# Kernel tuning notes

Hardware: AMD Instinct MI355X
Metric: run time of the kernel (lower is better)

Reference implementation:

```python
import math
import jax, jax.numpy as jnp
import numpy as np

D_MODEL = 1024
D_K = 64
D_V = 64
N_HEADS = 16
D_HIDDEN = 4096
EPS = 1e-5


def setup_inputs() -> dict:
    key = jax.random.key(0)
    ks = jax.random.split(key, 10)
    s = 0.02
    x = jax.random.normal(ks[0], (2, 2048, D_MODEL), dtype=jnp.float32)
    wq = jax.random.normal(ks[1], (D_MODEL, D_K * N_HEADS), jnp.float32) * s
    bq = jnp.zeros((D_K * N_HEADS,), jnp.float32)
    wk = jax.random.normal(ks[2], (D_MODEL, D_K * N_HEADS), jnp.float32) * s
    bk = jnp.zeros((D_K * N_HEADS,), jnp.float32)
    wv = jax.random.normal(ks[3], (D_MODEL, D_V * N_HEADS), jnp.float32) * s
    bv = jnp.zeros((D_V * N_HEADS,), jnp.float32)
    wo = jax.random.normal(ks[4], (D_V * N_HEADS, D_MODEL), jnp.float32) * s
    ln1_g = jnp.ones((D_MODEL,), jnp.float32)
    ln1_b = jnp.zeros((D_MODEL,), jnp.float32)
    w1 = jax.random.normal(ks[5], (D_MODEL, D_HIDDEN), jnp.float32) * s
    b1 = jnp.zeros((D_HIDDEN,), jnp.float32)
    w2 = jax.random.normal(ks[6], (D_HIDDEN, D_MODEL), jnp.float32) * s
    ln2_g = jnp.ones((D_MODEL,), jnp.float32)
    ln2_b = jnp.zeros((D_MODEL,), jnp.float32)
    return dict(x=x, wq=wq, bq=bq, wk=wk, bk=bk, wv=wv, bv=bv, wo=wo,
                ln1_g=ln1_g, ln1_b=ln1_b, w1=w1, b1=b1, w2=w2,
                ln2_g=ln2_g, ln2_b=ln2_b)


def _layernorm(x, g, b):
    mu = jnp.mean(x, axis=-1, keepdims=True)
    var = jnp.mean((x - mu) ** 2, axis=-1, keepdims=True)
    return (x - mu) * jax.lax.rsqrt(var + EPS) * g + b


def reference(x, wq, bq, wk, bk, wv, bv, wo, ln1_g, ln1_b, w1, b1, w2, ln2_g, ln2_b):
    B, S, _ = x.shape
    split = lambda t, d: t.reshape(B, S, N_HEADS, d).transpose(0, 2, 1, 3)  # [B,H,S,d]
    Q = split(x @ wq + bq, D_K)
    K = split(x @ wk + bk, D_K)
    V = split(x @ wv + bv, D_V)
    scores = jnp.einsum('bhqd,bhkd->bhqk', Q / math.sqrt(D_K), K)
    causal = jnp.tril(jnp.ones((S, S), dtype=bool))
    scores = jnp.where(causal, scores, -jnp.inf)
    attn = jax.nn.softmax(scores, axis=-1)
    ctx = jnp.einsum('bhqk,bhkd->bhqd', attn, V)  # [B,H,S,d_v]
    merged = ctx.transpose(0, 2, 1, 3).reshape(B, S, N_HEADS * D_V)
    x = x + _layernorm(merged @ wo, ln1_g, ln1_b)
    h = jax.nn.gelu(x @ w1 + b1, approximate=False)
    x = x + _layernorm(h @ w2, ln2_g, ln2_b)
    return x
```

## Files before the change

### kernel.cpp

```cpp
#include <hip/hip_runtime.h>
#include <math.h>

typedef __bf16 bf16;
typedef __bf16 bf16x4 __attribute__((ext_vector_type(4)));
typedef __bf16 bf16x8 __attribute__((ext_vector_type(8)));
typedef float f32x4 __attribute__((ext_vector_type(4)));

#define MFMA16(a, b, c) __builtin_amdgcn_mfma_f32_16x16x32_bf16(a, b, c, 0, 0, 0)
#define QSCALE 0.180336879f
#define SSTR 3072
#define SOFT_M -14.0f

typedef __attribute__((address_space(3))) unsigned int lds_uint;
typedef const __attribute__((address_space(1))) unsigned int glb_uint;
__device__ __forceinline__ void gload_lds16(const void* g, void* l) {
    __builtin_amdgcn_global_load_lds((glb_uint*)g, (lds_uint*)l, 16, 0, 0);
}
__device__ __forceinline__ unsigned lds_addr(const void* p) {
    return (unsigned)(unsigned long long)(lds_uint*)p;
}

__global__ __launch_bounds__(256) void prep_kernel(
    const float* __restrict__ x,
    const float* __restrict__ wq, const float* __restrict__ wk,
    const float* __restrict__ wv, const float* __restrict__ wo,
    const float* __restrict__ w1, const float* __restrict__ w2,
    const float* __restrict__ bq, const float* __restrict__ bk,
    const float* __restrict__ bv,
    bf16* __restrict__ xbf, bf16* __restrict__ wqkvt, bf16* __restrict__ wot,
    bf16* __restrict__ w1t, bf16* __restrict__ w2t, float* __restrict__ bqkv) {
    const int bid = blockIdx.x, tid = threadIdx.x;
    if (bid < 4096) {
        size_t i = ((size_t)bid * 256 + tid) * 4;
        float4 v = *(const float4*)(x + i);
        bf16x4 o = {(bf16)v.x, (bf16)v.y, (bf16)v.z, (bf16)v.w};
        *(bf16x4*)(xbf + i) = o;
        return;
    }
    if (bid < 16384) {
        __shared__ float tile[32][33];
        const float* W; bf16* Wt; int K, N, n0, k0;
        if (bid < 8192) {
            int l = bid - 4096, z = l >> 10, t = l & 1023;
            W = z == 0 ? wq : z == 1 ? wk : z == 2 ? wv : wo;
            Wt = z == 3 ? wot : wqkvt + (size_t)z * 1024 * 1024;
            K = 1024; N = 1024; n0 = (t & 31) * 32; k0 = (t >> 5) * 32;
        } else if (bid < 12288) {
            int l = bid - 8192;
            W = w1; Wt = w1t; K = 1024; N = 4096;
            n0 = (l & 127) * 32; k0 = (l >> 7) * 32;
        } else {
            int l = bid - 12288;
            W = w2; Wt = w2t; K = 4096; N = 1024;
            n0 = (l & 31) * 32; k0 = (l >> 5) * 32;
        }
        const int tx = tid & 31, ty = tid >> 5;
        for (int i = 0; i < 32; i += 8)
            tile[ty + i][tx] = W[(size_t)(k0 + ty + i) * N + n0 + tx];
        __syncthreads();
        for (int i = 0; i < 32; i += 8)
            Wt[(size_t)(n0 + ty + i) * K + k0 + tx] = (bf16)tile[tx][ty + i];
        return;
    }
    int i = (bid - 16384) * 256 + tid;
    bqkv[i] = i < 1024 ? bq[i] : i < 2048 ? bk[i - 1024] : bv[i - 2048];
}

__global__ void transpose_v_kernel(const bf16* __restrict__ QKV, bf16* __restrict__ Vtg) {
    __shared__ bf16 t[64 * 64];
    const int tid = threadIdx.x;
    const int st = blockIdx.x;
    const int bh = blockIdx.y;
    const int b = bh >> 4, h = bh & 15;
    const bf16* src = QKV + (size_t)b * 2048 * SSTR + 2048 + h * 64 + (size_t)st * 64 * SSTR;
    const int s = tid >> 3, oct = tid & 7;
    bf16x8 v0 = *(const bf16x8*)&src[(size_t)s * SSTR + oct * 8];
    bf16x8 v1 = *(const bf16x8*)&src[(size_t)(s + 32) * SSTR + oct * 8];
    *(bf16x8*)&t[s * 64 + ((oct ^ (s & 7)) * 8)] = v0;
    *(bf16x8*)&t[(s + 32) * 64 + ((oct ^ (s & 7)) * 8)] = v1;
    __syncthreads();
    const int dv = tid >> 3, so = tid & 7;
    bf16 b0[8], b1[8];
#pragma unroll
    for (int j = 0; j < 8; j++) {
        int ss = (so & 4) * 8 + (so & 3) * 4 + (j < 4 ? j : 12 + j);
        b0[j] = t[ss * 64 + (((dv >> 3) ^ (ss & 7)) * 8) + (dv & 7)];
        b1[j] = t[ss * 64 + ((((dv + 32) >> 3) ^ (ss & 7)) * 8) + (dv & 7)];
    }
    bf16* dst = Vtg + (size_t)bh * 64 * 2048 + (size_t)st * 64;
    *(bf16x8*)&dst[(size_t)dv * 2048 + so * 8] = *(bf16x8*)b0;
    *(bf16x8*)&dst[(size_t)(dv + 32) * 2048 + so * 8] = *(bf16x8*)b1;
}

template <bool HAS_BIAS, bool DO_GELU, bool OUT_BF16, bool QKV_SCALE, int NSPLIT>
__global__ __launch_bounds__(256, 4) void gemm_nt(
    const bf16* __restrict__ A, const bf16* __restrict__ Bt,
    const float* __restrict__ bias,
    float* __restrict__ Cf, bf16* __restrict__ Cb,
    int M, int N, int K) {
    __shared__ bf16 As[2][128 * 32];
    __shared__ bf16 Bs[2][128 * 32];
    const int tid = threadIdx.x;
    const int wave = tid >> 6, lane = tid & 63;
    const int ln = lane & 15, quad = lane >> 4;
    const int GN = N >> 7;
    const int nblk = gridDim.x;
    const int bid = blockIdx.x;
    const int lid = (bid & 7) * (nblk >> 3) + (bid >> 3);
    const int ngroup = GN * 8;
    const int g = lid / ngroup, rem = lid - g * ngroup;
    const int m0 = (g * 8 + (rem & 7)) * 128;
    const int n0 = (rem >> 3) * 128;
    const int wm = (wave >> 1) * 64, wn = (wave & 1) * 64;
    int kz0 = 0, kz1 = K;
    if (NSPLIT > 1) {
        const int kchunk = K / NSPLIT;
        kz0 = blockIdx.z * kchunk;
        kz1 = kz0 + kchunk;
        if (OUT_BF16) Cb += (size_t)blockIdx.z * M * N;
        else          Cf += (size_t)blockIdx.z * M * N;
    }
    const int srow0 = wave * 32 + (lane >> 2);
    const int srow1 = srow0 + 16;
    const int soct = ((lane & 3) ^ (srow0 & 3)) * 8;
    const bf16* ga0 = A + (size_t)(m0 + srow0) * K + soct;
    const bf16* ga1 = A + (size_t)(m0 + srow1) * K + soct;
    const bf16* gb0 = Bt + (size_t)(n0 + srow0) * K + soct;
    const bf16* gb1 = Bt + (size_t)(n0 + srow1) * K + soct;

    f32x4 acc[4][4] = {};
    const int roct = (quad ^ (ln & 3)) * 8;

#define GSTAGE(k0_, bi_)                                        \
    {                                                           \
        bf16* la = As[bi_] + wave * 1024;                       \
        bf16* lb = Bs[bi_] + wave * 1024;                       \
        gload_lds16(ga0 + (k0_), la);                           \
        gload_lds16(ga1 + (k0_), la + 512);                     \
        gload_lds16(gb0 + (k0_), lb);                           \
        gload_lds16(gb1 + (k0_), lb + 512);                     \
    }

    GSTAGE(kz0, 0)
    int it = 0;
    for (int k0 = kz0; k0 < kz1; k0 += 32, ++it) {
        const int cur = it & 1;
        __syncthreads();
        if (k0 + 32 < kz1) GSTAGE(k0 + 32, cur ^ 1)
        bf16x8 af[4], bg[4];
#pragma unroll
        for (int i = 0; i < 4; i++) {
            af[i] = *(const bf16x8*)&As[cur][(wm + i * 16 + ln) * 32 + roct];
            bg[i] = *(const bf16x8*)&Bs[cur][(wn + i * 16 + ln) * 32 + roct];
        }
#pragma unroll
        for (int i = 0; i < 4; i++)
#pragma unroll
            for (int j = 0; j < 4; j++)
                acc[i][j] = MFMA16(af[i], bg[j], acc[i][j]);
    }
#undef GSTAGE

#pragma unroll
    for (int i = 0; i < 4; i++)
#pragma unroll
        for (int j = 0; j < 4; j++) {
            int col = n0 + wn + j * 16 + ln;
            float bv = HAS_BIAS ? bias[col] : 0.0f;
#pragma unroll
            for (int r = 0; r < 4; r++) {
                int row = m0 + wm + i * 16 + quad * 4 + r;
                float v = acc[i][j][r] + bv;
                if (QKV_SCALE && col < 1024) v *= QSCALE;
                if (DO_GELU) {
                    float u = v * (v * v * 0.044715f + 1.0f) * 0.7978845608f;
                    float t = __builtin_amdgcn_exp2f(u * 2.885390082f);
                    v = v * t * __builtin_amdgcn_rcpf(t + 1.0f);
                }
                if (OUT_BF16)
                    Cb[(size_t)row * N + col] = (bf16)v;
                else
                    Cf[(size_t)row * N + col] = v;
            }
        }
}

#define BARR() __builtin_amdgcn_s_barrier()
#define WAITDS() { asm volatile("s_waitcnt lgkmcnt(0)" ::: "memory"); \
                   __builtin_amdgcn_sched_barrier(0); }
#define WAITVM8() asm volatile("s_waitcnt vmcnt(8)" ::: "memory")
#define WAITVM0() asm volatile("s_waitcnt vmcnt(0)" ::: "memory")
#define PRIO1() __builtin_amdgcn_s_setprio(1)
#define PRIO0() __builtin_amdgcn_s_setprio(0)
#define DSR(d_, a_, o_) asm volatile("ds_read_b128 %0, %1 offset:%2" \
                                     : "=v"(d_) : "v"(a_), "i"(o_))

__device__ __forceinline__ void mfma_q(f32x4 (&acc)[8][4], const bf16x8 (&aF)[4][2],
                                       const bf16x8 (&bR)[2][2], int IO, int NO) {
#pragma unroll
    for (int i = 0; i < 4; i++)
#pragma unroll
        for (int n = 0; n < 2; n++) {
            acc[IO + i][NO + n] = MFMA16(aF[i][0], bR[n][0], acc[IO + i][NO + n]);
            acc[IO + i][NO + n] = MFMA16(aF[i][1], bR[n][1], acc[IO + i][NO + n]);
        }
}

template <bool HAS_BIAS, bool DO_GELU, bool QKV_SCALE, int NSPLIT>
__global__ __launch_bounds__(512, 2) void gemm256(
    const bf16* __restrict__ A, const bf16* __restrict__ Bt,
    const float* __restrict__ bias, bf16* __restrict__ Cb,
    int M, int N, int K) {
    __shared__ bf16 sh[65536];
    const int tid = threadIdx.x;
    const int wave = tid >> 6, lane = tid & 63;
    const int ln = lane & 15, quad = lane >> 4;
    const int wm = (wave >> 2) * 128, wn = (wave & 3) * 64;
    const int GN = N >> 8;
    const int nblk = gridDim.x;
    const int bid = blockIdx.x;
    const int lid = (bid & 7) * (nblk >> 3) + (bid >> 3);
    const int ngroup = GN * 8;
    const int gg = lid / ngroup, rem = lid - gg * ngroup;
    const int m0 = (gg * 8 + (rem & 7)) * 256;
    const int n0 = (rem >> 3) * 256;
    int kz0 = 0, KS = K;
    if (NSPLIT > 1) {
        KS = K / NSPLIT;
        kz0 = blockIdx.z * KS;
        Cb += (size_t)blockIdx.z * M * N;
    }
    const int NT = KS >> 6;

    const int lr = lane >> 3, lc = lane & 7;
    const int co = (lc ^ lr) * 8;
    const int hg0 = wave * 16 + lr, hg1 = hg0 + 8;
    const int rA0g0 = hg0 + (hg0 >= 64 ? 64 : 0);
    const int rA0g1 = hg1 + (hg1 >= 64 ? 64 : 0);
    const int rB0g0 = (hg0 >> 5) * 64 + (hg0 & 31);
    const int rB0g1 = (hg1 >> 5) * 64 + (hg1 & 31);
    const bf16* gA0 = A + (size_t)(m0 + rA0g0) * K + kz0 + co;
    const bf16* gA1 = A + (size_t)(m0 + rA0g1) * K + kz0 + co;
    const bf16* gB0 = Bt + (size_t)(n0 + rB0g0) * K + kz0 + co;
    const bf16* gB1 = Bt + (size_t)(n0 + rB0g1) * K + kz0 + co;
    const size_t aoff64 = (size_t)64 * K;
    const size_t boff32 = (size_t)32 * K;
    const int hA0 = wave * 16, hA1 = wave * 16 + 8;
    const int R0A0 = hA0 + (hA0 >= 64 ? 64 : 0);
    const int R0A1 = hA1 + (hA1 >= 64 ? 64 : 0);
    const int R0B0 = (hA0 >> 5) * 64 + (hA0 & 31);
    const int R0B1 = (hA1 >> 5) * 64 + (hA1 & 31);

#define ST_A0(B_, T_) do { \
    gload_lds16(gA0 + (size_t)(T_) * 64, sh + (B_) * 16384 + R0A0 * 64); \
    gload_lds16(gA1 + (size_t)(T_) * 64, sh + (B_) * 16384 + R0A1 * 64); } while (0)
#define ST_A1(B_, T_) do { \
    gload_lds16(gA0 + aoff64 + (size_t)(T_) * 64, sh + (B_) * 16384 + 4096 + R0A0 * 64); \
    gload_lds16(gA1 + aoff64 + (size_t)(T_) * 64, sh + (B_) * 16384 + 4096 + R0A1 * 64); } while (0)
#define ST_B0(B_, T_) do { \
    gload_lds16(gB0 + (size_t)(T_) * 64, sh + 32768 + (B_) * 16384 + R0B0 * 64); \
    gload_lds16(gB1 + (size_t)(T_) * 64, sh + 32768 + (B_) * 16384 + R0B1 * 64); } while (0)
#define ST_B1(B_, T_) do { \
    gload_lds16(gB0 + boff32 + (size_t)(T_) * 64, sh + 32768 + (B_) * 16384 + 2048 + R0B0 * 64); \
    gload_lds16(gB1 + boff32 + (size_t)(T_) * 64, sh + 32768 + (B_) * 16384 + 2048 + R0B1 * 64); } while (0)

    const unsigned lb = lds_addr(sh);
    unsigned aAdr[2][2], bAdr[2][2];
#pragma unroll
    for (int bu = 0; bu < 2; bu++)
#pragma unroll
        for (int ks = 0; ks < 2; ks++) {
            unsigned sw = (unsigned)(((ks * 4 + quad) ^ (ln & 7)) * 16);
            aAdr[bu][ks] = lb + bu * 32768u + (unsigned)(wm + ln) * 128u + sw;
            bAdr[bu][ks] = lb + 65536u + bu * 32768u + (unsigned)(wn + ln) * 128u + sw;
        }

    f32x4 acc[8][4] = {};
    bf16x8 aF[4][2], bQ0[2][2], bQ1[2][2];

    ST_A0(0, 0); ST_B0(0, 0); ST_A1(0, 0); ST_B1(0, 0);
    ST_A0(1, 1); ST_B0(1, 1); ST_A1(1, 1); ST_B1(1, 1);
    WAITVM8();
    BARR();

#define TILE(B_, U_) { \
     \
    DSR(aF[0][0], aAdr[B_][0], 0);     DSR(aF[0][1], aAdr[B_][1], 0); \
    DSR(aF[1][0], aAdr[B_][0], 2048);  DSR(aF[1][1], aAdr[B_][1], 2048); \
    DSR(aF[2][0], aAdr[B_][0], 4096);  DSR(aF[2][1], aAdr[B_][1], 4096); \
    DSR(aF[3][0], aAdr[B_][0], 6144);  DSR(aF[3][1], aAdr[B_][1], 6144); \
    DSR(bQ0[0][0], bAdr[B_][0], 0);    DSR(bQ0[0][1], bAdr[B_][1], 0); \
    DSR(bQ0[1][0], bAdr[B_][0], 2048); DSR(bQ0[1][1], bAdr[B_][1], 2048); \
    BARR(); WAITDS(); PRIO1(); \
    mfma_q(acc, aF, bQ0, 0, 0); \
    PRIO0(); BARR(); \
     \
    DSR(bQ1[0][0], bAdr[B_][0], 4096); DSR(bQ1[0][1], bAdr[B_][1], 4096); \
    DSR(bQ1[1][0], bAdr[B_][0], 6144); DSR(bQ1[1][1], bAdr[B_][1], 6144); \
    if ((U_) + 2 < NT) { ST_A0(B_, (U_) + 2); ST_B0(B_, (U_) + 2); } \
    BARR(); WAITDS(); PRIO1(); \
    mfma_q(acc, aF, bQ1, 0, 2); \
    PRIO0(); BARR(); \
     \
    DSR(aF[0][0], aAdr[B_][0], 8192);  DSR(aF[0][1], aAdr[B_][1], 8192); \
    DSR(aF[1][0], aAdr[B_][0], 10240); DSR(aF[1][1], aAdr[B_][1], 10240); \
    DSR(aF[2][0], aAdr[B_][0], 12288); DSR(aF[2][1], aAdr[B_][1], 12288); \
    DSR(aF[3][0], aAdr[B_][0], 14336); DSR(aF[3][1], aAdr[B_][1], 14336); \
    if ((U_) + 2 < NT) ST_B1(B_, (U_) + 2); \
    BARR(); WAITDS(); PRIO1(); \
    mfma_q(acc, aF, bQ0, 4, 0); \
    PRIO0(); BARR(); \
     \
    if ((U_) + 2 < NT) ST_A1(B_, (U_) + 2); \
    if ((U_) >= NT - 2) { WAITVM0(); } else { WAITVM8(); } \
    BARR(); PRIO1(); \
    mfma_q(acc, aF, bQ1, 4, 2); \
    PRIO0(); BARR(); \
}

    for (int u = 0; u < NT; u += 2) {
        TILE(0, u)
        TILE(1, u + 1)
    }
#undef TILE
#undef ST_A0
#undef ST_A1
#undef ST_B0
#undef ST_B1

#pragma unroll
    for (int i = 0; i < 8; i++)
#pragma unroll
        for (int j = 0; j < 4; j++) {
            int col = n0 + wn + j * 16 + ln;
            float bvv = HAS_BIAS ? bias[col] : 0.0f;
#pragma unroll
            for (int rr = 0; rr < 4; rr++) {
                int row = m0 + wm + i * 16 + quad * 4 + rr;
                float v = acc[i][j][rr] + bvv;
                if (QKV_SCALE && col < 1024) v *= QSCALE;
                if (DO_GELU) {
                    float u = v * (v * v * 0.044715f + 1.0f) * 0.7978845608f;
                    float t = __builtin_amdgcn_exp2f(u * 2.885390082f);
                    v = v * t * __builtin_amdgcn_rcpf(t + 1.0f);
                }
                Cb[(size_t)row * N + col] = (bf16)v;
            }
        }
}

__global__ __launch_bounds__(256, 4) void attn_kernel(
    const bf16* __restrict__ QKV, const bf16* __restrict__ Vtg,
    bf16* __restrict__ ctx) {
    __shared__ bf16 Ks[2][64 * 64];
    __shared__ bf16 Vs[2][64 * 64];
    const int tid = threadIdx.x, wave = tid >> 6, lane = tid & 63;
    const int ln = lane & 15, quad = lane >> 4;
    const int idx = blockIdx.x;
    const int qt = 31 - (idx >> 5);
    const int bh = idx & 31;
    const int b = bh >> 4, h = bh & 15;
    const size_t qkvbase = (size_t)b * 2048 * SSTR;
    const bf16* Qp = QKV + qkvbase + h * 64;
    const bf16* Kp = QKV + qkvbase + 1024 + h * 64;
    const bf16* Vtp = Vtg + (size_t)bh * 64 * 2048;
    const int qw = qt * 64 + wave * 16;
    const int qg = qw + ln;

    bf16x8 bq0 = *(const bf16x8*)&Qp[(size_t)qg * SSTR + quad * 8];
    bf16x8 bq1 = *(const bf16x8*)&Qp[(size_t)qg * SSTR + 32 + quad * 8];

    f32x4 o[4] = {};
    float l_run = 0.0f;

    const int kr = wave * 16 + (lane >> 3);
    const int koct = ((lane & 7) ^ (kr & 7)) * 8;
    const bf16* gk0 = Kp + (size_t)kr * SSTR + koct;
    const bf16* gk1 = Kp + (size_t)(kr + 8) * SSTR + koct;
    const bf16* gv0 = Vtp + (size_t)kr * 2048 + koct;
    const bf16* gv1 = Vtp + (size_t)(kr + 8) * 2048 + koct;

    const int nkt = qt + 1;
#define STAGE(kt_, bi_)                                                     \
    {                                                                       \
        const int kk = (kt_) * 64;                                          \
        bf16* lk = Ks[bi_] + wave * 1024;                                   \
        bf16* lv = Vs[bi_] + wave * 1024;                                   \
        gload_lds16(gk0 + (size_t)kk * SSTR, lk);                           \
        gload_lds16(gk1 + (size_t)kk * SSTR, lk + 512);                     \
        gload_lds16(gv0 + kk, lv);                                          \
        gload_lds16(gv1 + kk, lv + 512);                                    \
    }

    STAGE(0, 0)
    for (int kt = 0; kt < nkt; kt++) {
        const int cur = kt & 1;
        const int k0 = kt * 64;
        __syncthreads();
        if (kt + 1 < nkt) STAGE(kt + 1, cur ^ 1)

        const bf16* Kc = Ks[cur];
        const bf16* Vc = Vs[cur];
        f32x4 sc[4];
#pragma unroll
        for (int mt = 0; mt < 4; mt++) {
            sc[mt][0] = SOFT_M; sc[mt][1] = SOFT_M;
            sc[mt][2] = SOFT_M; sc[mt][3] = SOFT_M;
        }
        __builtin_amdgcn_s_setprio(1);
#pragma unroll
        for (int mt = 0; mt < 4; mt++) {
            const int sk = mt * 16 + ln, s7 = sk & 7;
            bf16x8 ka0 = *(const bf16x8*)&Kc[sk * 64 + ((quad ^ s7) * 8)];
            bf16x8 ka1 = *(const bf16x8*)&Kc[sk * 64 + (((quad + 4) ^ s7) * 8)];
            sc[mt] = MFMA16(ka0, bq0, sc[mt]);
            sc[mt] = MFMA16(ka1, bq1, sc[mt]);
        }
        __builtin_amdgcn_s_setprio(0);
        if (kt == qt) {
#pragma unroll
            for (int mt = 0; mt < 4; mt++)
#pragma unroll
                for (int r = 0; r < 4; r++) {
                    const int kg = k0 + mt * 16 + quad * 4 + r;
                    if (kg > qg) sc[mt][r] = -__builtin_inff();
                }
        }
        float sum = 0.0f;
#pragma unroll
        for (int mt = 0; mt < 4; mt++)
#pragma unroll
            for (int r = 0; r < 4; r++) {
                float pv = __builtin_amdgcn_exp2f(sc[mt][r]);
                sc[mt][r] = pv;
                sum += pv;
            }
        l_run += sum;

        bf16x8 pb0, pb1;
#pragma unroll
        for (int r = 0; r < 4; r++) {
            pb0[r]     = (bf16)sc[0][r];
            pb0[r + 4] = (bf16)sc[1][r];
            pb1[r]     = (bf16)sc[2][r];
            pb1[r + 4] = (bf16)sc[3][r];
        }
        __builtin_amdgcn_s_setprio(1);
#pragma unroll
        for (int nt = 0; nt < 4; nt++) {
            const int row = nt * 16 + ln, r7 = row & 7;
            bf16x8 va0 = *(const bf16x8*)&Vc[row * 64 + ((quad ^ r7) * 8)];
            bf16x8 va1 = *(const bf16x8*)&Vc[row * 64 + (((quad + 4) ^ r7) * 8)];
            o[nt] = MFMA16(va0, pb0, o[nt]);
            o[nt] = MFMA16(va1, pb1, o[nt]);
        }
        __builtin_amdgcn_s_setprio(0);
    }
#undef STAGE

    __syncthreads();
    l_run += __shfl_xor(l_run, 16);
    l_run += __shfl_xor(l_run, 32);
    const float inv = 1.0f / l_run;

    bf16* Ob = Ks[0] + wave * 1024;
#pragma unroll
    for (int nt = 0; nt < 4; nt++)
#pragma unroll
        for (int r = 0; r < 4; r++) {
            const int dvh = 2 * nt + (quad >> 1);
            const int dlo = (quad & 1) * 4 + r;
            Ob[ln * 64 + ((dvh ^ (ln & 7)) * 8) + dlo] = (bf16)(o[nt][r] * inv);
        }
    bf16* ctxp = ctx + (size_t)b * 2048 * 1024 + h * 64;
#pragma unroll
    for (int p2 = 0; p2 < 2; p2++) {
        const int qL = (lane >> 3) + 8 * p2;
        const int oct = lane & 7;
        bf16x8 v = *(const bf16x8*)&Ob[qL * 64 + ((oct ^ (qL & 7)) * 8)];
        *(bf16x8*)&ctxp[(size_t)(qw + qL) * 1024 + oct * 8] = v;
    }
}

template <int NPART>
__global__ __launch_bounds__(256) void ln_res_kernel(
    const float* res, const bf16* __restrict__ yb,
    const float* __restrict__ g, const float* __restrict__ beta,
    float* outf, bf16* __restrict__ outb) {
    const int row = blockIdx.x;
    const int tid = threadIdx.x;
    const size_t off = (size_t)row * 1024 + tid * 4;
    const size_t pstride = (size_t)4096 * 1024;
    float4 v = {0.0f, 0.0f, 0.0f, 0.0f};
#pragma unroll
    for (int pi = 0; pi < NPART; pi++) {
        bf16x4 a = *(const bf16x4*)(yb + pi * pstride + off);
        v.x += (float)a[0]; v.y += (float)a[1];
        v.z += (float)a[2]; v.w += (float)a[3];
    }
    float s = v.x + v.y + v.z + v.w;
    float s2 = v.x * v.x + v.y * v.y + v.z * v.z + v.w * v.w;
#pragma unroll
    for (int o = 1; o < 64; o <<= 1) {
        s += __shfl_xor(s, o);
        s2 += __shfl_xor(s2, o);
    }
    __shared__ float ws[8];
    const int wave = tid >> 6, lane = tid & 63;
    if (lane == 0) { ws[wave] = s; ws[4 + wave] = s2; }
    __syncthreads();
    s = ws[0] + ws[1] + ws[2] + ws[3];
    s2 = ws[4] + ws[5] + ws[6] + ws[7];
    float mu = s * (1.0f / 1024.0f);
    float var = s2 * (1.0f / 1024.0f) - mu * mu;
    float rs = rsqrtf(var + 1e-5f);
    float4 gv = *(const float4*)(g + tid * 4);
    float4 bv = *(const float4*)(beta + tid * 4);
    float4 rv = *(const float4*)(res + off);
    float4 ov;
    ov.x = rv.x + (v.x - mu) * rs * gv.x + bv.x;
    ov.y = rv.y + (v.y - mu) * rs * gv.y + bv.y;
    ov.z = rv.z + (v.z - mu) * rs * gv.z + bv.z;
    ov.w = rv.w + (v.w - mu) * rs * gv.w + bv.w;
    *(float4*)(outf + off) = ov;
    if (outb) {
        bf16x4 ob = {(bf16)ov.x, (bf16)ov.y, (bf16)ov.z, (bf16)ov.w};
        *(bf16x4*)(outb + off) = ob;
    }
}


extern "C" void kernel_launch(void* const* d_in, const int* in_sizes, int n_in,
                              void* d_out, int out_size, void* d_ws, size_t ws_size,
                              hipStream_t stream) {
    const float* x  = (const float*)d_in[0];
    const float* wq = (const float*)d_in[1];
    const float* bq = (const float*)d_in[2];
    const float* wk = (const float*)d_in[3];
    const float* bk = (const float*)d_in[4];
    const float* wv = (const float*)d_in[5];
    const float* bv = (const float*)d_in[6];
    const float* wo = (const float*)d_in[7];
    const float* g1 = (const float*)d_in[8];
    const float* be1 = (const float*)d_in[9];
    const float* w1 = (const float*)d_in[10];
    const float* b1 = (const float*)d_in[11];
    const float* w2 = (const float*)d_in[12];
    const float* g2 = (const float*)d_in[13];
    const float* be2 = (const float*)d_in[14];
    float* out = (float*)d_out;

    const int T = 4096;
    char* p = (char*)d_ws;
    auto take = [&](size_t n) { char* r = p; p += n; return r; };
    bf16* xbf   = (bf16*)take((size_t)T * 1024 * 2);
    bf16* wqkvt = (bf16*)take((size_t)3072 * 1024 * 2);
    float* bqkv = (float*)take(3072 * 4 + 4096);
    bf16* wot   = (bf16*)take(1024 * 1024 * 2);
    bf16* w1t   = (bf16*)take((size_t)4096 * 1024 * 2);
    bf16* w2t   = (bf16*)take((size_t)1024 * 4096 * 2);
    bf16* QKV   = (bf16*)take((size_t)T * 3072 * 2);
    bf16* ctx   = (bf16*)take((size_t)T * 1024 * 2);
    bf16* ypart = (bf16*)take((size_t)2 * T * 1024 * 2);
    bf16* Vtg   = (bf16*)take((size_t)32 * 64 * 2048 * 2);
    take((size_t)T * 1024 * 2);
    bf16* h   = QKV;
    bf16* x1b = xbf;
    float* x1 = out;

    prep_kernel<<<16396, 256, 0, stream>>>(x, wq, wk, wv, wo, w1, w2, bq, bk, bv,
                                           xbf, wqkvt, wot, w1t, w2t, bqkv);

    gemm256<true, false, true, 1><<<192, 512, 0, stream>>>(
        xbf, wqkvt, bqkv, QKV, T, 3072, 1024);

    transpose_v_kernel<<<dim3(32, 32), 256, 0, stream>>>(QKV, Vtg);
    attn_kernel<<<1024, 256, 0, stream>>>(QKV, Vtg, ctx);

    gemm_nt<false, false, true, false, 2><<<dim3(256, 1, 2), 256, 0, stream>>>(
        ctx, wot, nullptr, nullptr, ypart, T, 1024, 1024);

    ln_res_kernel<2><<<T, 256, 0, stream>>>(x, ypart, g1, be1, x1, x1b);

    gemm256<true, true, false, 1><<<256, 512, 0, stream>>>(
        x1b, w1t, b1, h, T, 4096, 1024);

    gemm256<false, false, false, 4><<<dim3(64, 1, 4), 512, 0, stream>>>(
        h, w2t, nullptr, ypart, T, 1024, 4096);

    ln_res_kernel<4><<<T, 256, 0, stream>>>(x1, ypart, g2, be2, out, nullptr);
}
```

Measured before the change: 309.2 us.

## Restructure GEMM main loop to overlap LDS reads with MFMAs and cut barriers

Reworks the 256x256 bf16 GEMM inner loop so the next tile's first LDS fragment reads are issued at the end of the current tile. Partial lgkmcnt waits let MFMAs start as soon as each fragment group arrives, and the number of block barriers per tile drops from eight to three. The global-to-LDS prefetch order changes: A1 of the next buffer is loaded earlier and vmcnt thresholds are retuned. The aim is to hide LDS latency behind matrix ops. The cost is more complex hazard reasoning about buffer reuse and wait counts.

```diff
diff --git a/kernel.cpp b/kernel.cpp
--- a/kernel.cpp
+++ b/kernel.cpp
@@ -186,25 +186,19 @@
 }
 
 #define BARR() __builtin_amdgcn_s_barrier()
-#define WAITDS() { asm volatile("s_waitcnt lgkmcnt(0)" ::: "memory"); \
-                   __builtin_amdgcn_sched_barrier(0); }
-#define WAITVM8() asm volatile("s_waitcnt vmcnt(8)" ::: "memory")
-#define WAITVM0() asm volatile("s_waitcnt vmcnt(0)" ::: "memory")
+#define WAITLG(n_) { asm volatile("s_waitcnt lgkmcnt(" #n_ ")" ::: "memory"); \
+                     __builtin_amdgcn_sched_barrier(0); }
+#define WAITVM(n_) asm volatile("s_waitcnt vmcnt(" #n_ ")" ::: "memory")
 #define PRIO1() __builtin_amdgcn_s_setprio(1)
 #define PRIO0() __builtin_amdgcn_s_setprio(0)
 #define DSR(d_, a_, o_) asm volatile("ds_read_b128 %0, %1 offset:%2" \
                                      : "=v"(d_) : "v"(a_), "i"(o_))
 
-__device__ __forceinline__ void mfma_q(f32x4 (&acc)[8][4], const bf16x8 (&aF)[4][2],
-                                       const bf16x8 (&bR)[2][2], int IO, int NO) {
-#pragma unroll
-    for (int i = 0; i < 4; i++)
-#pragma unroll
-        for (int n = 0; n < 2; n++) {
-            acc[IO + i][NO + n] = MFMA16(aF[i][0], bR[n][0], acc[IO + i][NO + n]);
-            acc[IO + i][NO + n] = MFMA16(aF[i][1], bR[n][1], acc[IO + i][NO + n]);
-        }
-}
+#define MF4(i_, IO_, NO_, BQ_) { \
+    acc[(IO_) + (i_)][NO_] = MFMA16(aF[i_][0], BQ_[0][0], acc[(IO_) + (i_)][NO_]); \
+    acc[(IO_) + (i_)][NO_] = MFMA16(aF[i_][1], BQ_[0][1], acc[(IO_) + (i_)][NO_]); \
+    acc[(IO_) + (i_)][(NO_) + 1] = MFMA16(aF[i_][0], BQ_[1][0], acc[(IO_) + (i_)][(NO_) + 1]); \
+    acc[(IO_) + (i_)][(NO_) + 1] = MFMA16(aF[i_][1], BQ_[1][1], acc[(IO_) + (i_)][(NO_) + 1]); }
 
 template <bool HAS_BIAS, bool DO_GELU, bool QKV_SCALE, int NSPLIT>
 __global__ __launch_bounds__(512, 2) void gemm256(
@@ -278,44 +272,64 @@
     f32x4 acc[8][4] = {};
     bf16x8 aF[4][2], bQ0[2][2], bQ1[2][2];
 
-    ST_A0(0, 0); ST_B0(0, 0); ST_A1(0, 0); ST_B1(0, 0);
-    ST_A0(1, 1); ST_B0(1, 1); ST_A1(1, 1); ST_B1(1, 1);
-    WAITVM8();
-    BARR();
-
-#define TILE(B_, U_) { \
-     \
+#define RD_Q1(B_) { \
     DSR(aF[0][0], aAdr[B_][0], 0);     DSR(aF[0][1], aAdr[B_][1], 0); \
     DSR(aF[1][0], aAdr[B_][0], 2048);  DSR(aF[1][1], aAdr[B_][1], 2048); \
     DSR(aF[2][0], aAdr[B_][0], 4096);  DSR(aF[2][1], aAdr[B_][1], 4096); \
     DSR(aF[3][0], aAdr[B_][0], 6144);  DSR(aF[3][1], aAdr[B_][1], 6144); \
     DSR(bQ0[0][0], bAdr[B_][0], 0);    DSR(bQ0[0][1], bAdr[B_][1], 0); \
-    DSR(bQ0[1][0], bAdr[B_][0], 2048); DSR(bQ0[1][1], bAdr[B_][1], 2048); \
-    BARR(); WAITDS(); PRIO1(); \
-    mfma_q(acc, aF, bQ0, 0, 0); \
-    PRIO0(); BARR(); \
-     \
+    DSR(bQ0[1][0], bAdr[B_][0], 2048); DSR(bQ0[1][1], bAdr[B_][1], 2048); }
+#define RD_Q2(B_) { \
     DSR(bQ1[0][0], bAdr[B_][0], 4096); DSR(bQ1[0][1], bAdr[B_][1], 4096); \
-    DSR(bQ1[1][0], bAdr[B_][0], 6144); DSR(bQ1[1][1], bAdr[B_][1], 6144); \
-    if ((U_) + 2 < NT) { ST_A0(B_, (U_) + 2); ST_B0(B_, (U_) + 2); } \
-    BARR(); WAITDS(); PRIO1(); \
-    mfma_q(acc, aF, bQ1, 0, 2); \
-    PRIO0(); BARR(); \
-     \
+    DSR(bQ1[1][0], bAdr[B_][0], 6144); DSR(bQ1[1][1], bAdr[B_][1], 6144); }
+#define RD_Q3(B_) { \
     DSR(aF[0][0], aAdr[B_][0], 8192);  DSR(aF[0][1], aAdr[B_][1], 8192); \
     DSR(aF[1][0], aAdr[B_][0], 10240); DSR(aF[1][1], aAdr[B_][1], 10240); \
     DSR(aF[2][0], aAdr[B_][0], 12288); DSR(aF[2][1], aAdr[B_][1], 12288); \
-    DSR(aF[3][0], aAdr[B_][0], 14336); DSR(aF[3][1], aAdr[B_][1], 14336); \
+    DSR(aF[3][0], aAdr[B_][0], 14336); DSR(aF[3][1], aAdr[B_][1], 14336); }
+
+    ST_A0(0, 0); ST_B0(0, 0);
+    ST_B1(0, 0);
+    ST_A1(0, 0);
+    ST_A0(1, 1); ST_B0(1, 1);
+    ST_B1(1, 1);
+    WAITVM(6);
+    BARR();
+    RD_Q1(0);
+
+#define TILE(B_, U_) { \
+     \
+    RD_Q2(B_); \
+    WAITLG(4); PRIO1(); \
+    MF4(0, 0, 0, bQ0) MF4(1, 0, 0, bQ0) MF4(2, 0, 0, bQ0) MF4(3, 0, 0, bQ0) \
+    PRIO0(); \
+    BARR();   \
+     \
+    if ((U_) + 2 < NT) { ST_A0(B_, (U_) + 2); ST_B0(B_, (U_) + 2); } \
+    if ((U_) + 1 < NT) ST_A1((B_) ^ 1, (U_) + 1); \
+     \
+    WAITLG(0); PRIO1(); \
+    MF4(0, 0, 2, bQ1) MF4(1, 0, 2, bQ1) MF4(2, 0, 2, bQ1) MF4(3, 0, 2, bQ1) \
+    PRIO0(); \
+     \
+    if ((U_) < NT - 2) { WAITVM(6); } else { WAITVM(0); } \
+    BARR();   \
+     \
     if ((U_) + 2 < NT) ST_B1(B_, (U_) + 2); \
-    BARR(); WAITDS(); PRIO1(); \
-    mfma_q(acc, aF, bQ0, 4, 0); \
-    PRIO0(); BARR(); \
-     \
-    if ((U_) + 2 < NT) ST_A1(B_, (U_) + 2); \
-    if ((U_) >= NT - 2) { WAITVM0(); } else { WAITVM8(); } \
-    BARR(); PRIO1(); \
-    mfma_q(acc, aF, bQ1, 4, 2); \
-    PRIO0(); BARR(); \
+     \
+    RD_Q3(B_); \
+    WAITLG(6); PRIO1(); MF4(0, 4, 0, bQ0) PRIO0(); \
+    WAITLG(4); PRIO1(); MF4(1, 4, 0, bQ0) PRIO0(); \
+    WAITLG(2); PRIO1(); MF4(2, 4, 0, bQ0) PRIO0(); \
+    WAITLG(0); PRIO1(); MF4(3, 4, 0, bQ0) PRIO0(); \
+     \
+    if ((U_) < NT - 2) { WAITVM(8); } else { WAITVM(0); } \
+    BARR();   \
+     \
+    PRIO1(); \
+    MF4(0, 4, 2, bQ1) MF4(1, 4, 2, bQ1) MF4(2, 4, 2, bQ1) MF4(3, 4, 2, bQ1) \
+    PRIO0(); \
+    if ((U_) + 1 < NT) RD_Q1((B_) ^ 1); \
 }
 
     for (int u = 0; u < NT; u += 2) {
@@ -323,6 +337,9 @@
         TILE(1, u + 1)
     }
 #undef TILE
+#undef RD_Q1
+#undef RD_Q2
+#undef RD_Q3
 #undef ST_A0
 #undef ST_A1
 #undef ST_B0
```

Measured after the change: 315.9 us. 2.2% more time.

## Restructure gemm256 to 4 waves with 128x128 warp tiles and register double-buffering

Applied to the files above, without the earlier changes.

The 256x256 GEMM block now uses 4 waves of 256 threads instead of 8 waves of 512. Each wave computes a 128x128 sub-tile with a full 8x8 accumulator array, which raises the MFMA work per LDS fragment read. LDS reads for the next k-half are issued before the MFMAs that consume the current one, so fragment loads overlap compute and the number of barriers per tile drops. The cost is much higher register pressure (256 accumulator floats plus four fragment sets), only one block per CU, and fewer waves to hide latency.

```diff
diff --git a/kernel.cpp b/kernel.cpp
--- a/kernel.cpp
+++ b/kernel.cpp
@@ -186,28 +186,36 @@
 }
 
 #define BARR() __builtin_amdgcn_s_barrier()
-#define WAITDS() { asm volatile("s_waitcnt lgkmcnt(0)" ::: "memory"); \
-                   __builtin_amdgcn_sched_barrier(0); }
-#define WAITVM8() asm volatile("s_waitcnt vmcnt(8)" ::: "memory")
-#define WAITVM0() asm volatile("s_waitcnt vmcnt(0)" ::: "memory")
+#define WAITLG(n_) { asm volatile("s_waitcnt lgkmcnt(" #n_ ")" ::: "memory"); \
+                     __builtin_amdgcn_sched_barrier(0); }
+#define WAITVM(n_) asm volatile("s_waitcnt vmcnt(" #n_ ")" ::: "memory")
 #define PRIO1() __builtin_amdgcn_s_setprio(1)
 #define PRIO0() __builtin_amdgcn_s_setprio(0)
 #define DSR(d_, a_, o_) asm volatile("ds_read_b128 %0, %1 offset:%2" \
                                      : "=v"(d_) : "v"(a_), "i"(o_))
 
-__device__ __forceinline__ void mfma_q(f32x4 (&acc)[8][4], const bf16x8 (&aF)[4][2],
-                                       const bf16x8 (&bR)[2][2], int IO, int NO) {
-#pragma unroll
-    for (int i = 0; i < 4; i++)
-#pragma unroll
-        for (int n = 0; n < 2; n++) {
-            acc[IO + i][NO + n] = MFMA16(aF[i][0], bR[n][0], acc[IO + i][NO + n]);
-            acc[IO + i][NO + n] = MFMA16(aF[i][1], bR[n][1], acc[IO + i][NO + n]);
-        }
+__device__ __forceinline__ void rd8(bf16x8 (&R)[8], unsigned adr) {
+    DSR(R[0], adr, 0);     DSR(R[1], adr, 2048);
+    DSR(R[2], adr, 4096);  DSR(R[3], adr, 6144);
+    DSR(R[4], adr, 8192);  DSR(R[5], adr, 10240);
+    DSR(R[6], adr, 12288); DSR(R[7], adr, 14336);
+}
+__device__ __forceinline__ void stage8(const bf16* g, bf16* l, size_t row32K) {
+#pragma unroll
+    for (int rd = 0; rd < 8; rd++)
+        gload_lds16(g + (size_t)rd * row32K, l + rd * 2048);
+}
+__device__ __forceinline__ void burst32(f32x4 (&acc)[8][8], const bf16x8 (&aR)[8],
+                                        const bf16x8 (&bR)[8], int J0) {
+#pragma unroll
+    for (int i = 0; i < 8; i++)
+#pragma unroll
+        for (int j = 0; j < 4; j++)
+            acc[i][J0 + j] = MFMA16(aR[i], bR[J0 + j], acc[i][J0 + j]);
 }
 
 template <bool HAS_BIAS, bool DO_GELU, bool QKV_SCALE, int NSPLIT>
-__global__ __launch_bounds__(512, 2) void gemm256(
+__global__ __launch_bounds__(256, 1) void gemm256(
     const bf16* __restrict__ A, const bf16* __restrict__ Bt,
     const float* __restrict__ bias, bf16* __restrict__ Cb,
     int M, int N, int K) {
@@ -215,7 +223,7 @@
     const int tid = threadIdx.x;
     const int wave = tid >> 6, lane = tid & 63;
     const int ln = lane & 15, quad = lane >> 4;
-    const int wm = (wave >> 2) * 128, wn = (wave & 3) * 64;
+    const int wm = (wave >> 1) * 128, wn = (wave & 1) * 128;
     const int GN = N >> 8;
     const int nblk = gridDim.x;
     const int bid = blockIdx.x;
@@ -234,35 +242,14 @@
 
     const int lr = lane >> 3, lc = lane & 7;
     const int co = (lc ^ lr) * 8;
-    const int hg0 = wave * 16 + lr, hg1 = hg0 + 8;
-    const int rA0g0 = hg0 + (hg0 >= 64 ? 64 : 0);
-    const int rA0g1 = hg1 + (hg1 >= 64 ? 64 : 0);
-    const int rB0g0 = (hg0 >> 5) * 64 + (hg0 & 31);
-    const int rB0g1 = (hg1 >> 5) * 64 + (hg1 & 31);
-    const bf16* gA0 = A + (size_t)(m0 + rA0g0) * K + kz0 + co;
-    const bf16* gA1 = A + (size_t)(m0 + rA0g1) * K + kz0 + co;
-    const bf16* gB0 = Bt + (size_t)(n0 + rB0g0) * K + kz0 + co;
-    const bf16* gB1 = Bt + (size_t)(n0 + rB0g1) * K + kz0 + co;
-    const size_t aoff64 = (size_t)64 * K;
-    const size_t boff32 = (size_t)32 * K;
-    const int hA0 = wave * 16, hA1 = wave * 16 + 8;
-    const int R0A0 = hA0 + (hA0 >= 64 ? 64 : 0);
-    const int R0A1 = hA1 + (hA1 >= 64 ? 64 : 0);
-    const int R0B0 = (hA0 >> 5) * 64 + (hA0 & 31);
-    const int R0B1 = (hA1 >> 5) * 64 + (hA1 & 31);
-
-#define ST_A0(B_, T_) do { \
-    gload_lds16(gA0 + (size_t)(T_) * 64, sh + (B_) * 16384 + R0A0 * 64); \
-    gload_lds16(gA1 + (size_t)(T_) * 64, sh + (B_) * 16384 + R0A1 * 64); } while (0)
-#define ST_A1(B_, T_) do { \
-    gload_lds16(gA0 + aoff64 + (size_t)(T_) * 64, sh + (B_) * 16384 + 4096 + R0A0 * 64); \
-    gload_lds16(gA1 + aoff64 + (size_t)(T_) * 64, sh + (B_) * 16384 + 4096 + R0A1 * 64); } while (0)
-#define ST_B0(B_, T_) do { \
-    gload_lds16(gB0 + (size_t)(T_) * 64, sh + 32768 + (B_) * 16384 + R0B0 * 64); \
-    gload_lds16(gB1 + (size_t)(T_) * 64, sh + 32768 + (B_) * 16384 + R0B1 * 64); } while (0)
-#define ST_B1(B_, T_) do { \
-    gload_lds16(gB0 + boff32 + (size_t)(T_) * 64, sh + 32768 + (B_) * 16384 + 2048 + R0B0 * 64); \
-    gload_lds16(gB1 + boff32 + (size_t)(T_) * 64, sh + 32768 + (B_) * 16384 + 2048 + R0B1 * 64); } while (0)
+    const bf16* gA = A + (size_t)(m0 + wave * 8 + lr) * K + kz0 + co;
+    const bf16* gB = Bt + (size_t)(n0 + wave * 8 + lr) * K + kz0 + co;
+    const size_t row32K = (size_t)32 * K;
+    bf16* shA = sh + wave * 512;
+    bf16* shB = sh + 32768 + wave * 512;
+
+#define ST_A(B_, T_) stage8(gA + (size_t)(T_) * 64, shA + (B_) * 16384, row32K)
+#define ST_B(B_, T_) stage8(gB + (size_t)(T_) * 64, shB + (B_) * 16384, row32K)
 
     const unsigned lb = lds_addr(sh);
     unsigned aAdr[2][2], bAdr[2][2];
@@ -275,47 +262,30 @@
             bAdr[bu][ks] = lb + 65536u + bu * 32768u + (unsigned)(wn + ln) * 128u + sw;
         }
 
-    f32x4 acc[8][4] = {};
-    bf16x8 aF[4][2], bQ0[2][2], bQ1[2][2];
-
-    ST_A0(0, 0); ST_B0(0, 0); ST_A1(0, 0); ST_B1(0, 0);
-    ST_A0(1, 1); ST_B0(1, 1); ST_A1(1, 1); ST_B1(1, 1);
-    WAITVM8();
+    f32x4 acc[8][8] = {};
+    bf16x8 a0[8], b0[8], a1[8], b1[8];
+
+    ST_A(0, 0); ST_B(0, 0);
+    ST_A(1, 1); ST_B(1, 1);
+    WAITVM(16);
     BARR();
+    rd8(a0, aAdr[0][0]); rd8(b0, bAdr[0][0]);
 
 #define TILE(B_, U_) { \
-     \
-    DSR(aF[0][0], aAdr[B_][0], 0);     DSR(aF[0][1], aAdr[B_][1], 0); \
-    DSR(aF[1][0], aAdr[B_][0], 2048);  DSR(aF[1][1], aAdr[B_][1], 2048); \
-    DSR(aF[2][0], aAdr[B_][0], 4096);  DSR(aF[2][1], aAdr[B_][1], 4096); \
-    DSR(aF[3][0], aAdr[B_][0], 6144);  DSR(aF[3][1], aAdr[B_][1], 6144); \
-    DSR(bQ0[0][0], bAdr[B_][0], 0);    DSR(bQ0[0][1], bAdr[B_][1], 0); \
-    DSR(bQ0[1][0], bAdr[B_][0], 2048); DSR(bQ0[1][1], bAdr[B_][1], 2048); \
-    BARR(); WAITDS(); PRIO1(); \
-    mfma_q(acc, aF, bQ0, 0, 0); \
-    PRIO0(); BARR(); \
-     \
-    DSR(bQ1[0][0], bAdr[B_][0], 4096); DSR(bQ1[0][1], bAdr[B_][1], 4096); \
-    DSR(bQ1[1][0], bAdr[B_][0], 6144); DSR(bQ1[1][1], bAdr[B_][1], 6144); \
-    if ((U_) + 2 < NT) { ST_A0(B_, (U_) + 2); ST_B0(B_, (U_) + 2); } \
-    BARR(); WAITDS(); PRIO1(); \
-    mfma_q(acc, aF, bQ1, 0, 2); \
-    PRIO0(); BARR(); \
-     \
-    DSR(aF[0][0], aAdr[B_][0], 8192);  DSR(aF[0][1], aAdr[B_][1], 8192); \
-    DSR(aF[1][0], aAdr[B_][0], 10240); DSR(aF[1][1], aAdr[B_][1], 10240); \
-    DSR(aF[2][0], aAdr[B_][0], 12288); DSR(aF[2][1], aAdr[B_][1], 12288); \
-    DSR(aF[3][0], aAdr[B_][0], 14336); DSR(aF[3][1], aAdr[B_][1], 14336); \
-    if ((U_) + 2 < NT) ST_B1(B_, (U_) + 2); \
-    BARR(); WAITDS(); PRIO1(); \
-    mfma_q(acc, aF, bQ0, 4, 0); \
-    PRIO0(); BARR(); \
-     \
-    if ((U_) + 2 < NT) ST_A1(B_, (U_) + 2); \
-    if ((U_) >= NT - 2) { WAITVM0(); } else { WAITVM8(); } \
-    BARR(); PRIO1(); \
-    mfma_q(acc, aF, bQ1, 4, 2); \
-    PRIO0(); BARR(); \
+    rd8(a1, aAdr[B_][1]); rd8(b1, bAdr[B_][1]);    \
+    WAITLG(15); PRIO1(); \
+    burst32(acc, a0, b0, 0); burst32(acc, a0, b0, 4);   \
+    PRIO0(); WAITLG(0); PRIO1(); \
+    burst32(acc, a1, b1, 0);                            \
+    PRIO0(); \
+    BARR();   \
+    if ((U_) + 2 < NT) { ST_A(B_, (U_) + 2); ST_B(B_, (U_) + 2); } \
+    if ((U_) >= NT - 2) { WAITVM(0); } else { WAITVM(16); } \
+    BARR();   \
+    if ((U_) + 1 < NT) { rd8(a0, aAdr[(B_) ^ 1][0]); rd8(b0, bAdr[(B_) ^ 1][0]); } \
+    PRIO1(); \
+    burst32(acc, a1, b1, 4);                            \
+    PRIO0(); \
 }
 
     for (int u = 0; u < NT; u += 2) {
@@ -323,15 +293,13 @@
         TILE(1, u + 1)
     }
 #undef TILE
-#undef ST_A0
-#undef ST_A1
-#undef ST_B0
-#undef ST_B1
+#undef ST_A
+#undef ST_B
 
 #pragma unroll
     for (int i = 0; i < 8; i++)
 #pragma unroll
-        for (int j = 0; j < 4; j++) {
+        for (int j = 0; j < 8; j++) {
             int col = n0 + wn + j * 16 + ln;
             float bvv = HAS_BIAS ? bias[col] : 0.0f;
 #pragma unroll
@@ -571,7 +539,7 @@
     prep_kernel<<<16396, 256, 0, stream>>>(x, wq, wk, wv, wo, w1, w2, bq, bk, bv,
                                            xbf, wqkvt, wot, w1t, w2t, bqkv);
 
-    gemm256<true, false, true, 1><<<192, 512, 0, stream>>>(
+    gemm256<true, false, true, 1><<<192, 256, 0, stream>>>(
         xbf, wqkvt, bqkv, QKV, T, 3072, 1024);
 
     transpose_v_kernel<<<dim3(32, 32), 256, 0, stream>>>(QKV, Vtg);
@@ -582,10 +550,10 @@
 
     ln_res_kernel<2><<<T, 256, 0, stream>>>(x, ypart, g1, be1, x1, x1b);
 
-    gemm256<true, true, false, 1><<<256, 512, 0, stream>>>(
+    gemm256<true, true, false, 1><<<256, 256, 0, stream>>>(
         x1b, w1t, b1, h, T, 4096, 1024);
 
-    gemm256<false, false, false, 4><<<dim3(64, 1, 4), 512, 0, stream>>>(
+    gemm256<false, false, false, 4><<<dim3(64, 1, 4), 256, 0, stream>>>(
         h, w2t, nullptr, ypart, T, 1024, 4096);
 
     ln_res_kernel<4><<<T, 256, 0, stream>>>(x1, ypart, g2, be2, out, nullptr);
```

Result: slower. 495.1 us (+60.1%).
